# Kernel optimization log

Hardware: AMD Instinct MI355X
Metric: run time of the kernel (lower is better)

## Reference

```python
import jax, jax.numpy as jnp
import numpy as np

UNITS, N, S = 256, 64, 4
BATCH, T = 64, 1024


def setup_inputs() -> dict:
    key = jax.random.key(0)
    k0, k1, k2, k3 = jax.random.split(key, 4)
    return {
        "inputs": jax.random.uniform(k0, (BATCH, T, S), dtype=jnp.float32),
        "transition_kernel": jax.random.normal(k1, (UNITS, N, N), dtype=jnp.float32),
        "emission_kernel": jax.random.normal(k2, (UNITS, N, S), dtype=jnp.float32),
        "init_kernel": jax.random.normal(k3, (UNITS, N), dtype=jnp.float32),
    }


def reference(inputs, transition_kernel, emission_kernel, init_kernel):
    # Softmaxed HMM parameters (computed once; the TF cell recomputes per step).
    A = jax.nn.softmax(transition_kernel, axis=-1)  # [U, N, N] transitions
    B = jax.nn.softmax(emission_kernel, axis=-1)    # [U, N, S] emissions
    I = jax.nn.softmax(init_kernel, axis=-1)        # [U, N]    initial dist

    batch = inputs.shape[0]
    U, Nn = init_kernel.shape

    alpha0 = jnp.zeros((batch, U, Nn), dtype=inputs.dtype)
    ll0 = jnp.zeros((batch, U), dtype=inputs.dtype)
    is_init0 = jnp.ones((batch,), dtype=inputs.dtype)  # HMM starts in init at t=0

    def step(carry, x_t):
        alpha, ll, is_init = carry
        # R[b,u,j] = is_init[b]*I[u,j] + sum_i A[u,i,j]*alpha[b,u,i]  (A^T matvec)
        R = is_init[:, None, None] * I[None] + jnp.einsum("uij,bui->buj", A, alpha)
        # E[b,u,i] = sum_c B[u,i,c] * x_t[b,c]
        E = jnp.einsum("unc,bc->bun", B, x_t)
        fwd = E * R                              # [B, U, N]
        Ssum = jnp.sum(fwd, axis=-1)             # [B, U]
        ll = ll + jnp.log(Ssum)
        alpha = fwd / Ssum[..., None]            # normalized forward variable
        return (alpha, ll, jnp.zeros_like(is_init)), ll

    xs = jnp.swapaxes(inputs, 0, 1)  # [T, B, S]
    (_, _, _), lls = jax.lax.scan(step, (alpha0, ll0, is_init0), xs)
    # whole-sequence output: cumulative log-likelihood per step, [B, T, U]
    return jnp.swapaxes(lls, 0, 1)
```

## Files before the change

### kernel.cpp

```cpp
#include <hip/hip_runtime.h>


#define U_ 256
#define N_ 64
#define S_ 4
#define B_ 64
#define T_ 1024
#define ROWP 72
#define LN2F 0.69314718055994530942f

typedef __attribute__((ext_vector_type(8))) __bf16 bf16x8;
typedef __attribute__((ext_vector_type(4))) float floatx4;

__device__ __forceinline__ int sig(int jt, int m) {
    return 32 * (jt >> 1) + 4 * (jt & 1) + 8 * (m >> 2) + (m & 3);
}

__launch_bounds__(256, 1)
__global__ void hmm_fwd_kernel(const float* __restrict__ xg,
                               const float* __restrict__ trans,
                               const float* __restrict__ emis,
                               const float* __restrict__ initk,
                               float* __restrict__ out)
{
    __shared__ __bf16 AT[N_ * ROWP];
    __shared__ float BemS[N_][S_];
    __shared__ float IS[N_];

    const int bid = blockIdx.x;
    const int u = ((bid & 7) << 5) | (bid >> 3);
    const int tid = threadIdx.x;
    const int lane = tid & 63;
    const int w = tid >> 6;
    const int q = lane >> 4;
    const int l = lane & 15;

    if (tid < 64) {
        const float* rowp = trans + (u * N_ + tid) * N_;
        float v[N_];
        #pragma unroll
        for (int k = 0; k < 16; ++k) {
            floatx4 t4 = *(const floatx4*)(rowp + 4 * k);
            v[4*k] = t4.x; v[4*k+1] = t4.y; v[4*k+2] = t4.z; v[4*k+3] = t4.w;
        }
        float m = v[0];
        #pragma unroll
        for (int j = 1; j < N_; ++j) m = fmaxf(m, v[j]);
        float s = 0.f;
        #pragma unroll
        for (int j = 0; j < N_; ++j) { v[j] = __expf(v[j] - m); s += v[j]; }
        float inv = 1.0f / s;
        #pragma unroll
        for (int j = 0; j < N_; ++j) AT[j * ROWP + tid] = (__bf16)(v[j] * inv);
    } else if (tid < 128) {
        int n = tid - 64;
        floatx4 e4 = *(const floatx4*)(emis + (u * N_ + n) * S_);
        float m = fmaxf(fmaxf(e4.x, e4.y), fmaxf(e4.z, e4.w));
        float a = __expf(e4.x - m), b2 = __expf(e4.y - m);
        float c = __expf(e4.z - m), d = __expf(e4.w - m);
        float inv = 1.0f / (a + b2 + c + d);
        BemS[n][0] = a*inv; BemS[n][1] = b2*inv; BemS[n][2] = c*inv; BemS[n][3] = d*inv;
    } else if (tid < 192) {
        int j = tid - 128;
        float v = initk[u * N_ + j];
        float m = v;
        #pragma unroll
        for (int s = 1; s < 64; s <<= 1) m = fmaxf(m, __shfl_xor(m, s, 64));
        float e = __expf(v - m);
        float ssum = e;
        #pragma unroll
        for (int s = 1; s < 64; s <<= 1) ssum += __shfl_xor(ssum, s, 64);
        IS[j] = e / ssum;
    }
    __syncthreads();

    bf16x8 afrag[4][2];
    #pragma unroll
    for (int jt = 0; jt < 4; ++jt)
        #pragma unroll
        for (int kt = 0; kt < 2; ++kt)
            afrag[jt][kt] = *(const bf16x8*)&AT[sig(jt, l) * ROWP + 32*kt + 8*q];

    bf16x8 afragE[4];
    #pragma unroll
    for (int jt = 0; jt < 4; ++jt) {
        #pragma unroll
        for (int p = 0; p < 8; ++p) afragE[jt][p] = (__bf16)0.f;
        if (q == 0) {
            #pragma unroll
            for (int c = 0; c < 4; ++c)
                afragE[jt][c] = (__bf16)BemS[sig(jt, l)][c];
        }
    }

    bf16x8 onesf;
    #pragma unroll
    for (int p = 0; p < 8; ++p) onesf[p] = (__bf16)1.0f;

    floatx4 P0[4], P1[4];
    #pragma unroll
    for (int jt = 0; jt < 4; ++jt)
        #pragma unroll
        for (int r = 0; r < 4; ++r) {
            P0[jt][r] = IS[sig(jt, 4*q + r)];
            P1[jt][r] = 0.f;
        }

    __asm__ volatile("" ::: "memory");

    const int b = 16*w + l;
    const float* xin = xg + b * (T_ * S_);
    float* llout = out + (size_t)b * T_ * U_ + u;

    const floatx4 z = {0.f, 0.f, 0.f, 0.f};
    floatx4 Ev[4];
    floatx4 ssvA = z, ssvB = z;

    bf16x8 be;
    #pragma unroll
    for (int p = 0; p < 8; ++p) be[p] = (__bf16)0.f;

    {
        floatx4 x0 = *(const floatx4*)xin;
        be[0] = (__bf16)x0.x; be[1] = (__bf16)x0.y;
        be[2] = (__bf16)x0.z; be[3] = (__bf16)x0.w;
        #pragma unroll
        for (int jt = 0; jt < 4; ++jt)
            Ev[jt] = __builtin_amdgcn_mfma_f32_16x16x32_bf16(afragE[jt], be, z, 0, 0, 0);
    }
    floatx4 xvA[4], xvB[4];
    #pragma unroll
    for (int i = 0; i < 4; ++i)
        xvA[i] = *(const floatx4*)(xin + (1 + i) * S_);

    float hist[8];
    float ssf = 1.0f;
    float fcur = 1.0f;
    float Cacc = 0.f;
    float offacc = 0.f, sumk = 0.f;

    auto step = [&](const floatx4& xr, int slot, bool own, bool ownP, float fsc) {
        floatx4 Rv[4];
        #pragma unroll
        for (int jt = 0; jt < 4; ++jt) Rv[jt] = P0[jt] + P1[jt];

        {
            float ssp = ssvA[0] + ssvB[0];
            if (slot == 0) {
                hist[7] = ownP ? ssp : hist[7];
            } else {
                hist[slot - 1] = own ? ssp : hist[slot - 1];
                if (slot == 6) ssf = ssp;
            }
        }

        be[0] = (__bf16)xr.x; be[1] = (__bf16)xr.y;
        be[2] = (__bf16)xr.z; be[3] = (__bf16)xr.w;

        floatx4 gv[4];
        #pragma unroll
        for (int jt = 0; jt < 4; ++jt) gv[jt] = (Ev[jt] * Rv[jt]) * fsc;

        bf16x8 bf0, bf1;
        #pragma unroll
        for (int p = 0; p < 4; ++p) {
            bf0[p]     = (__bf16)gv[0][p];
            bf0[4 + p] = (__bf16)gv[1][p];
            bf1[p]     = (__bf16)gv[2][p];
            bf1[4 + p] = (__bf16)gv[3][p];
        }

        #pragma unroll
        for (int jt = 0; jt < 4; ++jt)
            P0[jt] = __builtin_amdgcn_mfma_f32_16x16x32_bf16(afrag[jt][0], bf0, z, 0, 0, 0);
        #pragma unroll
        for (int jt = 0; jt < 4; ++jt)
            P1[jt] = __builtin_amdgcn_mfma_f32_16x16x32_bf16(afrag[jt][1], bf1, z, 0, 0, 0);
        ssvA = __builtin_amdgcn_mfma_f32_16x16x32_bf16(onesf, bf0, z, 0, 0, 0);
        ssvB = __builtin_amdgcn_mfma_f32_16x16x32_bf16(onesf, bf1, z, 0, 0, 0);
        #pragma unroll
        for (int jt = 0; jt < 4; ++jt)
            Ev[jt] = __builtin_amdgcn_mfma_f32_16x16x32_bf16(afragE[jt], be, z, 0, 0, 0);
    };

    #pragma unroll 1
    for (int tb = 0; tb < T_; tb += 8) {
        const int oct = (tb >> 3) & 3;
        const bool own  = (q == oct);
        const bool ownP = (q == ((oct + 3) & 3));

        #pragma unroll
        for (int i = 0; i < 4; ++i) {
            int ti = tb + 5 + i; ti = (ti < T_) ? ti : T_ - 1;
            xvB[i] = *(const floatx4*)(xin + ti * S_);
        }

        step(xvA[0], 0, own, ownP, fcur);
        step(xvA[1], 1, own, ownP, 1.0f);
        step(xvA[2], 2, own, ownP, 1.0f);
        step(xvA[3], 3, own, ownP, 1.0f);

        #pragma unroll
        for (int i = 0; i < 4; ++i) {
            int ti = tb + 9 + i; ti = (ti < T_) ? ti : T_ - 1;
            xvA[i] = *(const floatx4*)(xin + ti * S_);
        }

        step(xvB[0], 4, own, ownP, 1.0f);
        step(xvB[1], 5, own, ownP, 1.0f);
        step(xvB[2], 6, own, ownP, 1.0f);
        step(xvB[3], 7, own, ownP, 1.0f);

        if (oct == 3) {
            float ssp = ssvA[0] + ssvB[0];
            hist[7] = own ? ssp : hist[7];
        }

        {
            unsigned eb = (__float_as_uint(ssf) >> 23) & 255u;
            fcur = __uint_as_float((254u - eb) << 23);
            float kf = (float)((int)eb - 127);
            offacc += (q > oct) ? kf : 0.f;
            sumk   += kf;
        }

        if (oct == 3) {
            float base = Cacc + LN2F * offacc;
            float* fp = llout + (size_t)(tb - 24 + 8 * q) * U_;
            #pragma unroll
            for (int k = 0; k < 8; ++k)
                fp[(size_t)k * U_] = __logf(hist[k]) + base;
            Cacc += LN2F * sumk;
            offacc = 0.f; sumk = 0.f;
        }
    }
}

extern "C" void kernel_launch(void* const* d_in, const int* in_sizes, int n_in,
                              void* d_out, int out_size, void* d_ws, size_t ws_size,
                              hipStream_t stream) {
    const float* xg    = (const float*)d_in[0];
    const float* trans = (const float*)d_in[1];
    const float* emis  = (const float*)d_in[2];
    const float* initk = (const float*)d_in[3];
    float* out = (float*)d_out;
    hipLaunchKernelGGL(hmm_fwd_kernel, dim3(U_), dim3(256), 0, stream,
                       xg, trans, emis, initk, out);
}
```

Before: 334.3 us.

## Split each batch group's state across two waves with LDS exchange per step

Doubles the block to 512 threads so each pair of waves shares one 16-batch group, with each wave owning half of the 64 hidden states (two of the four j-tiles). Each step, a wave writes its bf16 forward fragment to a double-buffered LDS array, hits a block-wide barrier, then reads its partner's fragment to finish the K reduction. This halves the serial MFMA chain per wave and raises wave-level parallelism. In exchange it adds an LDS round trip and a full block barrier on every one of the 1024 recurrent steps.

```diff
diff --git a/kernel.cpp b/kernel.cpp
--- a/kernel.cpp
+++ b/kernel.cpp
@@ -16,7 +16,7 @@
     return 32 * (jt >> 1) + 4 * (jt & 1) + 8 * (m >> 2) + (m & 3);
 }
 
-__launch_bounds__(256, 1)
+__launch_bounds__(512, 2)
 __global__ void hmm_fwd_kernel(const float* __restrict__ xg,
                                const float* __restrict__ trans,
                                const float* __restrict__ emis,
@@ -26,12 +26,15 @@
     __shared__ __bf16 AT[N_ * ROWP];
     __shared__ float BemS[N_][S_];
     __shared__ float IS[N_];
+    __align__(16) __shared__ __bf16 XFR[2][8][64][8];
 
     const int bid = blockIdx.x;
     const int u = ((bid & 7) << 5) | (bid >> 3);
     const int tid = threadIdx.x;
     const int lane = tid & 63;
     const int w = tid >> 6;
+    const int p = w & 1;
+    const int gidx = w >> 1;
     const int q = lane >> 4;
     const int l = lane & 15;
 
@@ -74,59 +77,59 @@
     }
     __syncthreads();
 
-    bf16x8 afrag[4][2];
-    #pragma unroll
-    for (int jt = 0; jt < 4; ++jt)
+    bf16x8 afrag[2][2];
+    #pragma unroll
+    for (int jtl = 0; jtl < 2; ++jtl)
         #pragma unroll
         for (int kt = 0; kt < 2; ++kt)
-            afrag[jt][kt] = *(const bf16x8*)&AT[sig(jt, l) * ROWP + 32*kt + 8*q];
-
-    bf16x8 afragE[4];
-    #pragma unroll
-    for (int jt = 0; jt < 4; ++jt) {
-        #pragma unroll
-        for (int p = 0; p < 8; ++p) afragE[jt][p] = (__bf16)0.f;
+            afrag[jtl][kt] = *(const bf16x8*)&AT[sig(2*p + jtl, l) * ROWP + 32*kt + 8*q];
+
+    bf16x8 afragE[2];
+    #pragma unroll
+    for (int jtl = 0; jtl < 2; ++jtl) {
+        #pragma unroll
+        for (int pp = 0; pp < 8; ++pp) afragE[jtl][pp] = (__bf16)0.f;
         if (q == 0) {
             #pragma unroll
             for (int c = 0; c < 4; ++c)
-                afragE[jt][c] = (__bf16)BemS[sig(jt, l)][c];
+                afragE[jtl][c] = (__bf16)BemS[sig(2*p + jtl, l)][c];
         }
     }
 
     bf16x8 onesf;
     #pragma unroll
-    for (int p = 0; p < 8; ++p) onesf[p] = (__bf16)1.0f;
-
-    floatx4 P0[4], P1[4];
-    #pragma unroll
-    for (int jt = 0; jt < 4; ++jt)
+    for (int pp = 0; pp < 8; ++pp) onesf[pp] = (__bf16)1.0f;
+
+    floatx4 Pown[2], Poth[2];
+    #pragma unroll
+    for (int jtl = 0; jtl < 2; ++jtl)
         #pragma unroll
         for (int r = 0; r < 4; ++r) {
-            P0[jt][r] = IS[sig(jt, 4*q + r)];
-            P1[jt][r] = 0.f;
+            Pown[jtl][r] = IS[sig(2*p + jtl, 4*q + r)];
+            Poth[jtl][r] = 0.f;
         }
 
     __asm__ volatile("" ::: "memory");
 
-    const int b = 16*w + l;
+    const int b = 16*gidx + l;
     const float* xin = xg + b * (T_ * S_);
     float* llout = out + (size_t)b * T_ * U_ + u;
 
     const floatx4 z = {0.f, 0.f, 0.f, 0.f};
-    floatx4 Ev[4];
-    floatx4 ssvA = z, ssvB = z;
+    floatx4 Ev[2];
+    floatx4 ssm = z, sso = z;
 
     bf16x8 be;
     #pragma unroll
-    for (int p = 0; p < 8; ++p) be[p] = (__bf16)0.f;
+    for (int pp = 0; pp < 8; ++pp) be[pp] = (__bf16)0.f;
 
     {
         floatx4 x0 = *(const floatx4*)xin;
         be[0] = (__bf16)x0.x; be[1] = (__bf16)x0.y;
         be[2] = (__bf16)x0.z; be[3] = (__bf16)x0.w;
         #pragma unroll
-        for (int jt = 0; jt < 4; ++jt)
-            Ev[jt] = __builtin_amdgcn_mfma_f32_16x16x32_bf16(afragE[jt], be, z, 0, 0, 0);
+        for (int jtl = 0; jtl < 2; ++jtl)
+            Ev[jtl] = __builtin_amdgcn_mfma_f32_16x16x32_bf16(afragE[jtl], be, z, 0, 0, 0);
     }
     floatx4 xvA[4], xvB[4];
     #pragma unroll
@@ -139,13 +142,13 @@
     float Cacc = 0.f;
     float offacc = 0.f, sumk = 0.f;
 
-    auto step = [&](const floatx4& xr, int slot, bool own, bool ownP, float fsc) {
-        floatx4 Rv[4];
-        #pragma unroll
-        for (int jt = 0; jt < 4; ++jt) Rv[jt] = P0[jt] + P1[jt];
-
+    __bf16* xfr_me = &XFR[0][w][lane][0];
+    const __bf16* xfr_pa = &XFR[0][w ^ 1][lane][0];
+    const int bufoff = 8 * 64 * 8;
+
+    auto step = [&](const floatx4& xr, int slot, bool own, bool ownP, float fsc, int buf) {
         {
-            float ssp = ssvA[0] + ssvB[0];
+            float ssp = ssm[0] + sso[0];
             if (slot == 0) {
                 hist[7] = ownP ? ssp : hist[7];
             } else {
@@ -154,33 +157,39 @@
             }
         }
 
+        floatx4 Rv[2];
+        #pragma unroll
+        for (int jtl = 0; jtl < 2; ++jtl) Rv[jtl] = Pown[jtl] + Poth[jtl];
+
+        floatx4 gv[2];
+        #pragma unroll
+        for (int jtl = 0; jtl < 2; ++jtl) gv[jtl] = (Ev[jtl] * Rv[jtl]) * fsc;
+
+        bf16x8 bfm;
+        #pragma unroll
+        for (int pp = 0; pp < 4; ++pp) {
+            bfm[pp]     = (__bf16)gv[0][pp];
+            bfm[4 + pp] = (__bf16)gv[1][pp];
+        }
+
         be[0] = (__bf16)xr.x; be[1] = (__bf16)xr.y;
         be[2] = (__bf16)xr.z; be[3] = (__bf16)xr.w;
 
-        floatx4 gv[4];
-        #pragma unroll
-        for (int jt = 0; jt < 4; ++jt) gv[jt] = (Ev[jt] * Rv[jt]) * fsc;
-
-        bf16x8 bf0, bf1;
-        #pragma unroll
-        for (int p = 0; p < 4; ++p) {
-            bf0[p]     = (__bf16)gv[0][p];
-            bf0[4 + p] = (__bf16)gv[1][p];
-            bf1[p]     = (__bf16)gv[2][p];
-            bf1[4 + p] = (__bf16)gv[3][p];
-        }
-
-        #pragma unroll
-        for (int jt = 0; jt < 4; ++jt)
-            P0[jt] = __builtin_amdgcn_mfma_f32_16x16x32_bf16(afrag[jt][0], bf0, z, 0, 0, 0);
-        #pragma unroll
-        for (int jt = 0; jt < 4; ++jt)
-            P1[jt] = __builtin_amdgcn_mfma_f32_16x16x32_bf16(afrag[jt][1], bf1, z, 0, 0, 0);
-        ssvA = __builtin_amdgcn_mfma_f32_16x16x32_bf16(onesf, bf0, z, 0, 0, 0);
-        ssvB = __builtin_amdgcn_mfma_f32_16x16x32_bf16(onesf, bf1, z, 0, 0, 0);
-        #pragma unroll
-        for (int jt = 0; jt < 4; ++jt)
-            Ev[jt] = __builtin_amdgcn_mfma_f32_16x16x32_bf16(afragE[jt], be, z, 0, 0, 0);
+        *(bf16x8*)(xfr_me + buf * bufoff) = bfm;
+        __asm__ volatile("s_waitcnt lgkmcnt(0)\n\ts_barrier" ::: "memory");
+        bf16x8 bfo = *(const bf16x8*)(xfr_pa + buf * bufoff);
+
+        #pragma unroll
+        for (int jtl = 0; jtl < 2; ++jtl)
+            Ev[jtl] = __builtin_amdgcn_mfma_f32_16x16x32_bf16(afragE[jtl], be, z, 0, 0, 0);
+        #pragma unroll
+        for (int jtl = 0; jtl < 2; ++jtl)
+            Pown[jtl] = __builtin_amdgcn_mfma_f32_16x16x32_bf16(afrag[jtl][p], bfm, z, 0, 0, 0);
+        ssm = __builtin_amdgcn_mfma_f32_16x16x32_bf16(onesf, bfm, z, 0, 0, 0);
+        #pragma unroll
+        for (int jtl = 0; jtl < 2; ++jtl)
+            Poth[jtl] = __builtin_amdgcn_mfma_f32_16x16x32_bf16(afrag[jtl][1 - p], bfo, z, 0, 0, 0);
+        sso = __builtin_amdgcn_mfma_f32_16x16x32_bf16(onesf, bfo, z, 0, 0, 0);
     };
 
     #pragma unroll 1
@@ -195,10 +204,10 @@
             xvB[i] = *(const floatx4*)(xin + ti * S_);
         }
 
-        step(xvA[0], 0, own, ownP, fcur);
-        step(xvA[1], 1, own, ownP, 1.0f);
-        step(xvA[2], 2, own, ownP, 1.0f);
-        step(xvA[3], 3, own, ownP, 1.0f);
+        step(xvA[0], 0, own, ownP, fcur, 0);
+        step(xvA[1], 1, own, ownP, 1.0f, 1);
+        step(xvA[2], 2, own, ownP, 1.0f, 0);
+        step(xvA[3], 3, own, ownP, 1.0f, 1);
 
         #pragma unroll
         for (int i = 0; i < 4; ++i) {
@@ -206,13 +215,13 @@
             xvA[i] = *(const floatx4*)(xin + ti * S_);
         }
 
-        step(xvB[0], 4, own, ownP, 1.0f);
-        step(xvB[1], 5, own, ownP, 1.0f);
-        step(xvB[2], 6, own, ownP, 1.0f);
-        step(xvB[3], 7, own, ownP, 1.0f);
+        step(xvB[0], 4, own, ownP, 1.0f, 0);
+        step(xvB[1], 5, own, ownP, 1.0f, 1);
+        step(xvB[2], 6, own, ownP, 1.0f, 0);
+        step(xvB[3], 7, own, ownP, 1.0f, 1);
 
         if (oct == 3) {
-            float ssp = ssvA[0] + ssvB[0];
+            float ssp = ssm[0] + sso[0];
             hist[7] = own ? ssp : hist[7];
         }
 
@@ -226,10 +235,12 @@
 
         if (oct == 3) {
             float base = Cacc + LN2F * offacc;
-            float* fp = llout + (size_t)(tb - 24 + 8 * q) * U_;
-            #pragma unroll
-            for (int k = 0; k < 8; ++k)
-                fp[(size_t)k * U_] = __logf(hist[k]) + base;
+            if ((q & 1) == p) {
+                float* fp = llout + (size_t)(tb - 24 + 8 * q) * U_;
+                #pragma unroll
+                for (int k = 0; k < 8; ++k)
+                    fp[(size_t)k * U_] = __logf(hist[k]) + base;
+            }
             Cacc += LN2F * sumk;
             offacc = 0.f; sumk = 0.f;
         }
@@ -244,6 +255,6 @@
     const float* emis  = (const float*)d_in[2];
     const float* initk = (const float*)d_in[3];
     float* out = (float*)d_out;
-    hipLaunchKernelGGL(hmm_fwd_kernel, dim3(U_), dim3(256), 0, stream,
+    hipLaunchKernelGGL(hmm_fwd_kernel, dim3(U_), dim3(512), 0, stream,
                        xg, trans, emis, initk, out);
 }
```

New measurement: 434.0 us. 1.3x slower.

## Halve batch columns per wave, double waves, compute row sums via shuffles

Applied to the files above, without the earlier changes.

Launches 512 threads per block so each wave handles 8 batch columns instead of 16. The unused MFMA columns (lanes with l>=8) are zeroed and their stores are masked. This gives more waves per CU to hide the latency of the serial MFMA dependency chain. The normalizer sum now comes from a VALU reduction plus cross-quad shuffles instead of two extra ones-vector MFMAs, which takes those MFMAs off the critical path. In exchange, half of each MFMA's columns do no useful work and twice as many waves compete for the matrix units.

```diff
diff --git a/kernel.cpp b/kernel.cpp
--- a/kernel.cpp
+++ b/kernel.cpp
@@ -16,7 +16,7 @@
     return 32 * (jt >> 1) + 4 * (jt & 1) + 8 * (m >> 2) + (m & 3);
 }
 
-__launch_bounds__(256, 1)
+__launch_bounds__(512, 2)
 __global__ void hmm_fwd_kernel(const float* __restrict__ xg,
                                const float* __restrict__ trans,
                                const float* __restrict__ emis,
@@ -34,6 +34,7 @@
     const int w = tid >> 6;
     const int q = lane >> 4;
     const int l = lane & 15;
+    const bool lval = (l < 8);
 
     if (tid < 64) {
         const float* rowp = trans + (u * N_ + tid) * N_;
@@ -85,7 +86,7 @@
     #pragma unroll
     for (int jt = 0; jt < 4; ++jt) {
         #pragma unroll
-        for (int p = 0; p < 8; ++p) afragE[jt][p] = (__bf16)0.f;
+        for (int pp = 0; pp < 8; ++pp) afragE[jt][pp] = (__bf16)0.f;
         if (q == 0) {
             #pragma unroll
             for (int c = 0; c < 4; ++c)
@@ -93,32 +94,27 @@
         }
     }
 
-    bf16x8 onesf;
-    #pragma unroll
-    for (int p = 0; p < 8; ++p) onesf[p] = (__bf16)1.0f;
-
     floatx4 P0[4], P1[4];
     #pragma unroll
     for (int jt = 0; jt < 4; ++jt)
         #pragma unroll
         for (int r = 0; r < 4; ++r) {
-            P0[jt][r] = IS[sig(jt, 4*q + r)];
+            P0[jt][r] = lval ? IS[sig(jt, 4*q + r)] : 0.f;
             P1[jt][r] = 0.f;
         }
 
     __asm__ volatile("" ::: "memory");
 
-    const int b = 16*w + l;
+    const int b = 8 * w + (l & 7);
     const float* xin = xg + b * (T_ * S_);
     float* llout = out + (size_t)b * T_ * U_ + u;
 
     const floatx4 z = {0.f, 0.f, 0.f, 0.f};
     floatx4 Ev[4];
-    floatx4 ssvA = z, ssvB = z;
 
     bf16x8 be;
     #pragma unroll
-    for (int p = 0; p < 8; ++p) be[p] = (__bf16)0.f;
+    for (int pp = 0; pp < 8; ++pp) be[pp] = (__bf16)0.f;
 
     {
         floatx4 x0 = *(const floatx4*)xin;
@@ -136,51 +132,54 @@
     float hist[8];
     float ssf = 1.0f;
     float fcur = 1.0f;
+    float pp0 = 0.f, pa16 = 0.f, pa32 = 0.f, pa48 = 0.f;
     float Cacc = 0.f;
     float offacc = 0.f, sumk = 0.f;
 
+    auto consume = [&](int kprev, bool o) {
+        float ss = (pp0 + pa16) + (pa32 + pa48);
+        hist[kprev] = o ? ss : hist[kprev];
+        if (kprev == 5) ssf = ss;
+    };
+
     auto step = [&](const floatx4& xr, int slot, bool own, bool ownP, float fsc) {
-        floatx4 Rv[4];
-        #pragma unroll
-        for (int jt = 0; jt < 4; ++jt) Rv[jt] = P0[jt] + P1[jt];
-
-        {
-            float ssp = ssvA[0] + ssvB[0];
-            if (slot == 0) {
-                hist[7] = ownP ? ssp : hist[7];
-            } else {
-                hist[slot - 1] = own ? ssp : hist[slot - 1];
-                if (slot == 6) ssf = ssp;
-            }
+        floatx4 gv[4];
+        #pragma unroll
+        for (int jt = 0; jt < 4; ++jt) {
+            floatx4 Rv = P0[jt] + P1[jt];
+            gv[jt] = (Ev[jt] * Rv) * fsc;
+        }
+
+        bf16x8 bf0, bf1;
+        #pragma unroll
+        for (int pp = 0; pp < 4; ++pp) {
+            bf0[pp]     = (__bf16)gv[0][pp];
+            bf0[4 + pp] = (__bf16)gv[1][pp];
+            bf1[pp]     = (__bf16)gv[2][pp];
+            bf1[4 + pp] = (__bf16)gv[3][pp];
         }
 
         be[0] = (__bf16)xr.x; be[1] = (__bf16)xr.y;
         be[2] = (__bf16)xr.z; be[3] = (__bf16)xr.w;
 
-        floatx4 gv[4];
-        #pragma unroll
-        for (int jt = 0; jt < 4; ++jt) gv[jt] = (Ev[jt] * Rv[jt]) * fsc;
-
-        bf16x8 bf0, bf1;
-        #pragma unroll
-        for (int p = 0; p < 4; ++p) {
-            bf0[p]     = (__bf16)gv[0][p];
-            bf0[4 + p] = (__bf16)gv[1][p];
-            bf1[p]     = (__bf16)gv[2][p];
-            bf1[4 + p] = (__bf16)gv[3][p];
-        }
-
         #pragma unroll
         for (int jt = 0; jt < 4; ++jt)
             P0[jt] = __builtin_amdgcn_mfma_f32_16x16x32_bf16(afrag[jt][0], bf0, z, 0, 0, 0);
         #pragma unroll
         for (int jt = 0; jt < 4; ++jt)
             P1[jt] = __builtin_amdgcn_mfma_f32_16x16x32_bf16(afrag[jt][1], bf1, z, 0, 0, 0);
-        ssvA = __builtin_amdgcn_mfma_f32_16x16x32_bf16(onesf, bf0, z, 0, 0, 0);
-        ssvB = __builtin_amdgcn_mfma_f32_16x16x32_bf16(onesf, bf1, z, 0, 0, 0);
+
+        if (slot == 0) consume(7, ownP); else consume(slot - 1, own);
+
         #pragma unroll
         for (int jt = 0; jt < 4; ++jt)
             Ev[jt] = __builtin_amdgcn_mfma_f32_16x16x32_bf16(afragE[jt], be, z, 0, 0, 0);
+
+        floatx4 s4 = (gv[0] + gv[1]) + (gv[2] + gv[3]);
+        pp0  = (s4.x + s4.y) + (s4.z + s4.w);
+        pa16 = __shfl_xor(pp0, 16, 64);
+        pa32 = __shfl_xor(pp0, 32, 64);
+        pa48 = __shfl_xor(pp0, 48, 64);
     };
 
     #pragma unroll 1
@@ -211,10 +210,7 @@
         step(xvB[2], 6, own, ownP, 1.0f);
         step(xvB[3], 7, own, ownP, 1.0f);
 
-        if (oct == 3) {
-            float ssp = ssvA[0] + ssvB[0];
-            hist[7] = own ? ssp : hist[7];
-        }
+        if (oct == 3) consume(7, own);
 
         {
             unsigned eb = (__float_as_uint(ssf) >> 23) & 255u;
@@ -226,10 +222,12 @@
 
         if (oct == 3) {
             float base = Cacc + LN2F * offacc;
-            float* fp = llout + (size_t)(tb - 24 + 8 * q) * U_;
-            #pragma unroll
-            for (int k = 0; k < 8; ++k)
-                fp[(size_t)k * U_] = __logf(hist[k]) + base;
+            if (lval) {
+                float* fp = llout + (size_t)(tb - 24 + 8 * q) * U_;
+                #pragma unroll
+                for (int k = 0; k < 8; ++k)
+                    fp[(size_t)k * U_] = __logf(hist[k]) + base;
+            }
             Cacc += LN2F * sumk;
             offacc = 0.f; sumk = 0.f;
         }
@@ -244,6 +242,6 @@
     const float* emis  = (const float*)d_in[2];
     const float* initk = (const float*)d_in[3];
     float* out = (float*)d_out;
-    hipLaunchKernelGGL(hmm_fwd_kernel, dim3(U_), dim3(256), 0, stream,
+    hipLaunchKernelGGL(hmm_fwd_kernel, dim3(U_), dim3(512), 0, stream,
                        xg, trans, emis, initk, out);
 }
```

After: 472.6 us. 41.4% more time.
